# Optimization experiments

Hardware: AMD Instinct MI355X
Metric: run time of the kernel (lower is better)

Reference implementation:

```python
import jax, jax.numpy as jnp
import numpy as np

B, T, D, H, FF = 4, 2048, 1024, 16, 4096
HD = D // H
EPS = 1e-5


def layernorm(x, g, b):
    m = jnp.mean(x, axis=-1, keepdims=True)
    v = jnp.var(x, axis=-1, keepdims=True)
    return (x - m) * jax.lax.rsqrt(v + EPS) * g + b


def setup_inputs() -> dict:
    key = jax.random.key(0)
    ks = jax.random.split(key, 12)
    s = lambda fan_in: 1.0 / np.sqrt(fan_in)
    x = jax.random.normal(ks[0], (B, T, D), dtype=jnp.float32)
    mask = jnp.tril(jnp.ones((T, T), dtype=jnp.int32))[None, None]  # [1,1,T,T] causal
    return {
        "x": x,
        "mask": mask,
        "ln1_g": jnp.ones((D,), jnp.float32),
        "ln1_b": jnp.zeros((D,), jnp.float32),
        "ln2_g": jnp.ones((D,), jnp.float32),
        "ln2_b": jnp.zeros((D,), jnp.float32),
        "qkv_w": jax.random.normal(ks[1], (D, 3 * D), jnp.float32) * s(D),
        "out_w": jax.random.normal(ks[2], (D, D), jnp.float32) * s(D),
        "out_b": jnp.zeros((D,), jnp.float32),
        "fc1_w": jax.random.normal(ks[3], (D, FF), jnp.float32) * s(D),
        "fc1_b": jnp.zeros((FF,), jnp.float32),
        "fc2_w": jax.random.normal(ks[4], (FF, D), jnp.float32) * s(FF),
        "fc2_b": jnp.zeros((D,), jnp.float32),
    }


def reference(x, mask, ln1_g, ln1_b, ln2_g, ln2_b, qkv_w, out_w, out_b,
              fc1_w, fc1_b, fc2_w, fc2_b):
    # --- attention sublayer (pre-LN) ---
    h = layernorm(x, ln1_g, ln1_b)
    qkv = h @ qkv_w  # [B,T,3D]
    q, k, v = jnp.split(qkv, 3, axis=-1)
    q = q.reshape(B, T, H, HD).transpose(0, 2, 1, 3)  # [B,H,T,hd]
    k = k.reshape(B, T, H, HD).transpose(0, 2, 1, 3)
    v = v.reshape(B, T, H, HD).transpose(0, 2, 1, 3)
    scale = 1.0 / np.sqrt(HD)
    scores = jnp.einsum('bhqd,bhkd->bhqk', q, k) * scale  # [B,H,T,T]
    scores = jnp.where(mask == 0, -jnp.inf, scores)
    attn = jax.nn.softmax(scores, axis=-1)
    o = jnp.einsum('bhqk,bhkd->bhqd', attn, v)
    o = o.transpose(0, 2, 1, 3).reshape(B, T, D)
    x = x + (o @ out_w + out_b)
    # --- MLP sublayer (pre-LN) ---
    h = layernorm(x, ln2_g, ln2_b)
    h = jax.nn.gelu(h @ fc1_w + fc1_b, approximate=False)
    x = x + (h @ fc2_w + fc2_b)
    return x
```

## Files before the change

### kernel.cpp

```cpp
#include <hip/hip_runtime.h>

typedef unsigned short bfraw;
typedef __attribute__((ext_vector_type(8))) short short8;
typedef __attribute__((ext_vector_type(4))) float f32x4;

__device__ __forceinline__ float b2f(bfraw u){ return __uint_as_float(((unsigned int)u)<<16); }
__device__ __forceinline__ bfraw f2b(float f){
  unsigned int u = __float_as_uint(f);
  return (bfraw)((u + 0x7FFFu + ((u>>16)&1u)) >> 16);
}
__device__ __forceinline__ void store_out(float* p, float v){ *p = v; }
__device__ __forceinline__ void store_out(bfraw* p, float v){ *p = f2b(v); }
__device__ __forceinline__ void gload_lds16(const bfraw* g, short* l) {
  __builtin_amdgcn_global_load_lds((const __attribute__((address_space(1))) void*)g,
                                   (__attribute__((address_space(3))) void*)l, 16, 0, 0);
}
__device__ __forceinline__ unsigned int cvt_pk_bf16(float a, float b) {
  unsigned int r;
  asm("v_cvt_pk_bf16_f32 %0, %1, %2" : "=v"(r) : "v"(a), "v"(b));
  return r;
}

__global__ __launch_bounds__(1024) void transpose_f32_bf16(const float* __restrict__ in,
                                                           bfraw* __restrict__ out,
                                                           int R, int C) {
  __shared__ bfraw tile[64][65];
  const int tx = threadIdx.x, ty = threadIdx.y;
  const int c0 = blockIdx.x*64, r0 = blockIdx.y*64;
  #pragma unroll
  for (int u = 0; u < 4; ++u)
    tile[ty + u*16][tx] = f2b(in[(size_t)(r0 + ty + u*16)*C + c0 + tx]);
  __syncthreads();
  #pragma unroll
  for (int u = 0; u < 4; ++u)
    out[(size_t)(c0 + ty + u*16)*R + r0 + tx] = tile[tx][ty + u*16];
}

__global__ __launch_bounds__(256) void ln_kernel(const float* __restrict__ x,
                                                 const float* __restrict__ g,
                                                 const float* __restrict__ b,
                                                 bfraw* __restrict__ out) {
  const int row = blockIdx.x, tid = threadIdx.x;
  const f32x4 v = ((const f32x4*)(x + (size_t)row*1024))[tid];
  float s  = v[0]+v[1]+v[2]+v[3];
  float s2 = v[0]*v[0]+v[1]*v[1]+v[2]*v[2]+v[3]*v[3];
  #pragma unroll
  for (int off = 1; off < 64; off <<= 1) { s += __shfl_xor(s, off); s2 += __shfl_xor(s2, off); }
  __shared__ float red[8];
  const int wv = tid>>6, ln_ = tid&63;
  if (ln_ == 0) { red[wv] = s; red[4+wv] = s2; }
  __syncthreads();
  float a  = red[0]+red[1]+red[2]+red[3];
  float a2 = red[4]+red[5]+red[6]+red[7];
  float mean = a*(1.0f/1024.0f);
  float var  = a2*(1.0f/1024.0f) - mean*mean;
  float inv  = rsqrtf(var + 1e-5f);
  const f32x4 gr = ((const f32x4*)g)[tid];
  const f32x4 br = ((const f32x4*)b)[tid];
  ushort4 o4;
  o4.x = f2b((v[0]-mean)*inv*gr[0] + br[0]);
  o4.y = f2b((v[1]-mean)*inv*gr[1] + br[1]);
  o4.z = f2b((v[2]-mean)*inv*gr[2] + br[2]);
  o4.w = f2b((v[3]-mean)*inv*gr[3] + br[3]);
  ((ushort4*)(out + (size_t)row*1024))[tid] = o4;
}

template<int EPI, typename OutT>
__global__ __launch_bounds__(256) void gemm_bt(const bfraw* __restrict__ A,
                                               const bfraw* __restrict__ Bt,
                                               const float* __restrict__ bias,
                                               const float* __restrict__ resid,
                                               OutT* __restrict__ C,
                                               int M, int N, int K) {
  __shared__ __align__(16) short As[128*32];
  __shared__ __align__(16) short Bs[128*32];
  const int tid = threadIdx.x;
  const int wave = tid>>6, lane = tid&63;
  const int wm = wave>>1, wn = wave&1;
  const int q = lane>>4, r = lane&15;
  const int bm = blockIdx.x, bn = blockIdx.y;

  const int m0 = tid>>2, c0 = tid&3;
  const bfraw* Ag0 = A  + (size_t)(bm*128      + m0)*K + c0*8;
  const bfraw* Ag1 = A  + (size_t)(bm*128 + 64 + m0)*K + c0*8;
  const bfraw* Bg0 = Bt + (size_t)(bn*128      + m0)*K + c0*8;
  const bfraw* Bg1 = Bt + (size_t)(bn*128 + 64 + m0)*K + c0*8;
  short* Al0 = &As[tid*8];
  short* Al1 = &As[(256+tid)*8];
  short* Bl0 = &Bs[tid*8];
  short* Bl1 = &Bs[(256+tid)*8];

  f32x4 acc[4][4];
  #pragma unroll
  for (int mi = 0; mi < 4; ++mi)
    #pragma unroll
    for (int ni = 0; ni < 4; ++ni)
      acc[mi][ni] = (f32x4){0.f, 0.f, 0.f, 0.f};

  for (int k0 = 0; k0 < K; k0 += 32) {
    __syncthreads();
    gload_lds16(Ag0 + k0, Al0);
    gload_lds16(Ag1 + k0, Al1);
    gload_lds16(Bg0 + k0, Bl0);
    gload_lds16(Bg1 + k0, Bl1);
    __syncthreads();
    short8 af[4], bfr[4];
    #pragma unroll
    for (int mi = 0; mi < 4; ++mi)
      af[mi] = *(const short8*)&As[(wm*64 + mi*16 + r)*32 + q*8];
    #pragma unroll
    for (int ni = 0; ni < 4; ++ni)
      bfr[ni] = *(const short8*)&Bs[(wn*64 + ni*16 + r)*32 + q*8];
    #pragma unroll
    for (int mi = 0; mi < 4; ++mi)
      #pragma unroll
      for (int ni = 0; ni < 4; ++ni)
        acc[mi][ni] = __builtin_amdgcn_mfma_f32_16x16x32_bf16(af[mi], bfr[ni], acc[mi][ni], 0, 0, 0);
  }

  #pragma unroll
  for (int mi = 0; mi < 4; ++mi) {
    #pragma unroll
    for (int ni = 0; ni < 4; ++ni) {
      const int gcol = bn*128 + wn*64 + ni*16 + r;
      float bv = 0.f;
      if constexpr (EPI != 0) bv = bias[gcol];
      #pragma unroll
      for (int rg = 0; rg < 4; ++rg) {
        const int grow = bm*128 + wm*64 + mi*16 + q*4 + rg;
        float val = acc[mi][ni][rg];
        if constexpr (EPI != 0) val += bv;
        if constexpr (EPI == 2) val = 0.5f*val*(1.0f + erff(val*0.70710678118654752f));
        if constexpr (EPI == 1) val += resid[(size_t)grow*N + gcol];
        store_out(&C[(size_t)grow*N + gcol], val);
      }
    }
  }
}

__global__ __launch_bounds__(256) void flash_attn(const bfraw* __restrict__ qkv,
                                                  bfraw* __restrict__ o) {
  __shared__ __align__(16) short Ksh[4096];
  __shared__ __align__(16) short Vts[4096];
  __shared__ __align__(16) short Psh[4096];
  const int tid = threadIdx.x;
  const int w = tid >> 6, lane = tid & 63;
  const int r = lane & 15, qd = lane >> 4;
  const int bb = blockIdx.y >> 4, h = blockIdx.y & 15;
  const size_t hb = (size_t)bb * 2048;
  short* Pw = &Psh[w * 1024];
  const int f0 = tid, f1 = tid + 256;
  const int key0 = f0 >> 3, dc0 = (f0 & 7) * 8;
  const int key1 = f1 >> 3, dc1 = (f1 & 7) * 8;

  for (int pass = 0; pass < 2; ++pass) {
    const int qt = pass ? (31 - (int)blockIdx.x) : (int)blockIdx.x;
    const int q0 = qt * 64;
    const int ntile = qt + 1;

    short8 qf[2];
    {
      const bfraw* qrow = qkv + (hb + q0 + w*16 + r) * 3072 + h*64;
      qf[0] = *(const short8*)(qrow + qd*8);
      qf[1] = *(const short8*)(qrow + qd*8 + 32);
    }

    f32x4 oacc[4];
    #pragma unroll
    for (int nt = 0; nt < 4; ++nt) oacc[nt] = (f32x4){0.f,0.f,0.f,0.f};
    float m_i = -3.0e38f;
    float l_i = 0.f;

    short8 kpre[2], vpre[2];
    {
      const bfraw* b0 = qkv + (hb + key0) * 3072 + h*64 + dc0;
      const bfraw* b1 = qkv + (hb + key1) * 3072 + h*64 + dc1;
      kpre[0] = *(const short8*)(b0 + 1024); vpre[0] = *(const short8*)(b0 + 2048);
      kpre[1] = *(const short8*)(b1 + 1024); vpre[1] = *(const short8*)(b1 + 2048);
    }

    for (int t = 0; t < ntile; ++t) {
      __syncthreads();
      #pragma unroll
      for (int pz = 0; pz < 2; ++pz) {
        const int key = pz ? key1 : key0, dc = pz ? dc1 : dc0;
        *(short8*)&Ksh[key*64 + ((((dc>>3) ^ (key>>3)) & 7) << 3)] = kpre[pz];
        const int kg = key >> 3, k7 = key & 7, dg = dc >> 3;
        #pragma unroll
        for (int i2 = 0; i2 < 8; ++i2)
          Vts[(dc + i2)*64 + (((kg ^ dg) & 7) << 3) + k7] = vpre[pz][i2];
      }
      __syncthreads();
      if (t + 1 < ntile) {
        const int j0n = (t + 1) * 64;
        const bfraw* b0 = qkv + (hb + j0n + key0) * 3072 + h*64 + dc0;
        const bfraw* b1 = qkv + (hb + j0n + key1) * 3072 + h*64 + dc1;
        kpre[0] = *(const short8*)(b0 + 1024); vpre[0] = *(const short8*)(b0 + 2048);
        kpre[1] = *(const short8*)(b1 + 1024); vpre[1] = *(const short8*)(b1 + 2048);
      }

      f32x4 s4[4];
      __builtin_amdgcn_s_setprio(1);
      #pragma unroll
      for (int kt = 0; kt < 4; ++kt) {
        f32x4 a = (f32x4){0.f,0.f,0.f,0.f};
        const int key = kt*16 + r, kgk = key >> 3;
        #pragma unroll
        for (int ks = 0; ks < 2; ++ks) {
          short8 kf8 = *(const short8*)&Ksh[key*64 + ((((qd + ks*4) ^ kgk) & 7) << 3)];
          a = __builtin_amdgcn_mfma_f32_16x16x32_bf16(kf8, qf[ks], a, 0, 0, 0);
        }
        s4[kt] = a;
      }
      __builtin_amdgcn_s_setprio(0);

      const bool diag = (t == qt);
      #pragma unroll
      for (int kt = 0; kt < 4; ++kt)
        #pragma unroll
        for (int rg = 0; rg < 4; ++rg) {
          float v = s4[kt][rg] * 0.125f;
          if (diag && (kt*16 + qd*4 + rg > w*16 + r)) v = -3.0e38f;
          s4[kt][rg] = v;
        }

      float mx = s4[0][0];
      #pragma unroll
      for (int kt = 0; kt < 4; ++kt)
        #pragma unroll
        for (int rg = 0; rg < 4; ++rg) mx = fmaxf(mx, s4[kt][rg]);
      mx = fmaxf(mx, __shfl_xor(mx, 16));
      mx = fmaxf(mx, __shfl_xor(mx, 32));
      const float mn = fmaxf(m_i, mx);
      const float alpha = __expf(m_i - mn);
      m_i = mn;
      l_i *= alpha;

      float lsum = 0.f;
      #pragma unroll
      for (int kt = 0; kt < 4; ++kt) {
        const float p0 = __expf(s4[kt][0] - mn);
        const float p1 = __expf(s4[kt][1] - mn);
        const float p2 = __expf(s4[kt][2] - mn);
        const float p3 = __expf(s4[kt][3] - mn);
        lsum += (p0 + p1) + (p2 + p3);
        uint2 pk;
        pk.x = cvt_pk_bf16(p0, p1);
        pk.y = cvt_pk_bf16(p2, p3);
        *(uint2*)((char*)Pw + r*128 + ((((kt*2 + (qd>>1)) ^ (r&7)) & 7) << 4) + ((qd&1)<<3)) = pk;
      }
      lsum += __shfl_xor(lsum, 16);
      lsum += __shfl_xor(lsum, 32);
      l_i += lsum;
      #pragma unroll
      for (int nt = 0; nt < 4; ++nt)
        #pragma unroll
        for (int rg = 0; rg < 4; ++rg) oacc[nt][rg] *= alpha;

      short8 pf[2];
      #pragma unroll
      for (int ks = 0; ks < 2; ++ks)
        pf[ks] = *(const short8*)&Pw[r*64 + ((((qd + ks*4) ^ (r & 7)) & 7) << 3)];
      __builtin_amdgcn_s_setprio(1);
      #pragma unroll
      for (int nt = 0; nt < 4; ++nt) {
        const int d = nt*16 + r, dg = d >> 3;
        #pragma unroll
        for (int ks = 0; ks < 2; ++ks) {
          short8 vf = *(const short8*)&Vts[d*64 + ((((qd + ks*4) ^ dg) & 7) << 3)];
          oacc[nt] = __builtin_amdgcn_mfma_f32_16x16x32_bf16(vf, pf[ks], oacc[nt], 0, 0, 0);
        }
      }
      __builtin_amdgcn_s_setprio(0);
    }

    const float invl = 1.0f / l_i;
    bfraw* orow = o + (hb + q0 + w*16 + r) * 1024 + h*64;
    #pragma unroll
    for (int nt = 0; nt < 4; ++nt) {
      uint2 ov;
      ov.x = cvt_pk_bf16(oacc[nt][0]*invl, oacc[nt][1]*invl);
      ov.y = cvt_pk_bf16(oacc[nt][2]*invl, oacc[nt][3]*invl);
      *(uint2*)(orow + nt*16 + qd*4) = ov;
    }
  }
}

extern "C" void kernel_launch(void* const* d_in, const int* in_sizes, int n_in,
                              void* d_out, int out_size, void* d_ws, size_t ws_size,
                              hipStream_t stream) {
  (void)in_sizes; (void)n_in;
  const float* x    = (const float*)d_in[0];
  const float* ln1g = (const float*)d_in[2];
  const float* ln1b = (const float*)d_in[3];
  const float* ln2g = (const float*)d_in[4];
  const float* ln2b = (const float*)d_in[5];
  const float* qkvw = (const float*)d_in[6];
  const float* outw = (const float*)d_in[7];
  const float* outb = (const float*)d_in[8];
  const float* fc1w = (const float*)d_in[9];
  const float* fc1b = (const float*)d_in[10];
  const float* fc2w = (const float*)d_in[11];
  const float* fc2b = (const float*)d_in[12];
  float* out = (float*)d_out;

  char* ws = (char*)d_ws;
  size_t off = 0;
  auto alloc = [&](size_t bytes) -> void* { void* p = ws + off; off += (bytes + 255) & ~(size_t)255; return p; };
  bfraw* wt_qkv = (bfraw*)alloc(3072ULL*1024*2);
  bfraw* wt_out = (bfraw*)alloc(1024ULL*1024*2);
  bfraw* wt_fc1 = (bfraw*)alloc(4096ULL*1024*2);
  bfraw* wt_fc2 = (bfraw*)alloc(1024ULL*4096*2);
  bfraw* hbuf   = (bfraw*)alloc(8192ULL*1024*2);
  float* x1     = (float*)alloc(8192ULL*1024*4);
  char*  big    = (char*) alloc(8192ULL*3072*2 + 8192ULL*1024*2);
  bfraw* qkv  = (bfraw*)big;
  bfraw* obuf = (bfraw*)(big + 8192ULL*3072*2);
  bfraw* hf   = (bfraw*)big;

  if (off > ws_size) {
    (void)hipMemsetAsync(d_out, 0x7F, (size_t)out_size*4, stream);
    return;
  }

  dim3 tb(64, 16);
  transpose_f32_bf16<<<dim3(48, 16), tb, 0, stream>>>(qkvw, wt_qkv, 1024, 3072);
  transpose_f32_bf16<<<dim3(16, 16), tb, 0, stream>>>(outw, wt_out, 1024, 1024);
  transpose_f32_bf16<<<dim3(64, 16), tb, 0, stream>>>(fc1w, wt_fc1, 1024, 4096);
  transpose_f32_bf16<<<dim3(16, 64), tb, 0, stream>>>(fc2w, wt_fc2, 4096, 1024);

  ln_kernel<<<8192, 256, 0, stream>>>(x, ln1g, ln1b, hbuf);
  gemm_bt<0, bfraw><<<dim3(64, 24), 256, 0, stream>>>(hbuf, wt_qkv, nullptr, nullptr, qkv, 8192, 3072, 1024);
  flash_attn<<<dim3(16, 64), 256, 0, stream>>>(qkv, obuf);
  gemm_bt<1, float><<<dim3(64, 8), 256, 0, stream>>>(obuf, wt_out, outb, x, x1, 8192, 1024, 1024);
  ln_kernel<<<8192, 256, 0, stream>>>(x1, ln2g, ln2b, hbuf);
  gemm_bt<2, bfraw><<<dim3(64, 32), 256, 0, stream>>>(hbuf, wt_fc1, fc1b, nullptr, hf, 8192, 4096, 1024);
  gemm_bt<1, float><<<dim3(64, 8), 256, 0, stream>>>(hf, wt_fc2, fc2b, x1, out, 8192, 1024, 4096);
}
```

Measured before the change: 591.4 us.

## Replace GEMM with 256x256 double-buffered, swizzled, prefetching MFMA kernel

Replaces the 128x128 single-buffered GEMM with a 256x256-tile kernel that uses 512 threads, double-buffered LDS holding 64-wide K chunks, XOR-swizzled LDS layout and a block-id remap across 8 groups. Global-to-LDS loads for the next tile are issued between MFMA phases, with vmcnt waits and raised wave priority during MFMA, so memory latency overlaps with compute. Larger tiles raise data reuse, but grid sizes become small (128 blocks for the N=1024 GEMMs), which may leave CUs idle, and LDS use per block grows considerably.

```diff
diff --git a/kernel.cpp b/kernel.cpp
--- a/kernel.cpp
+++ b/kernel.cpp
@@ -19,6 +19,13 @@
   unsigned int r;
   asm("v_cvt_pk_bf16_f32 %0, %1, %2" : "=v"(r) : "v"(a), "v"(b));
   return r;
+}
+__device__ __forceinline__ void waitvm4(){ asm volatile("s_waitcnt vmcnt(4)" ::: "memory"); }
+__device__ __forceinline__ void waitvm0(){ asm volatile("s_waitcnt vmcnt(0)" ::: "memory"); }
+__device__ __forceinline__ void fence_bar(){
+  __builtin_amdgcn_sched_barrier(0);
+  __builtin_amdgcn_s_barrier();
+  __builtin_amdgcn_sched_barrier(0);
 }
 
 __global__ __launch_bounds__(1024) void transpose_f32_bf16(const float* __restrict__ in,
@@ -66,68 +73,149 @@
 }
 
 template<int EPI, typename OutT>
-__global__ __launch_bounds__(256) void gemm_bt(const bfraw* __restrict__ A,
-                                               const bfraw* __restrict__ Bt,
-                                               const float* __restrict__ bias,
-                                               const float* __restrict__ resid,
-                                               OutT* __restrict__ C,
-                                               int M, int N, int K) {
-  __shared__ __align__(16) short As[128*32];
-  __shared__ __align__(16) short Bs[128*32];
+__global__ __launch_bounds__(512, 2) void gemm256(const bfraw* __restrict__ A,
+                                                  const bfraw* __restrict__ Bt,
+                                                  const float* __restrict__ bias,
+                                                  const float* __restrict__ resid,
+                                                  OutT* __restrict__ C,
+                                                  int M, int N, int K) {
+  __shared__ __align__(16) short As[2*2*8192];
+  __shared__ __align__(16) short Bs[2*2*8192];
   const int tid = threadIdx.x;
-  const int wave = tid>>6, lane = tid&63;
-  const int wm = wave>>1, wn = wave&1;
-  const int q = lane>>4, r = lane&15;
-  const int bm = blockIdx.x, bn = blockIdx.y;
-
-  const int m0 = tid>>2, c0 = tid&3;
-  const bfraw* Ag0 = A  + (size_t)(bm*128      + m0)*K + c0*8;
-  const bfraw* Ag1 = A  + (size_t)(bm*128 + 64 + m0)*K + c0*8;
-  const bfraw* Bg0 = Bt + (size_t)(bn*128      + m0)*K + c0*8;
-  const bfraw* Bg1 = Bt + (size_t)(bn*128 + 64 + m0)*K + c0*8;
-  short* Al0 = &As[tid*8];
-  short* Al1 = &As[(256+tid)*8];
-  short* Bl0 = &Bs[tid*8];
-  short* Bl1 = &Bs[(256+tid)*8];
-
-  f32x4 acc[4][4];
+  const int wv = tid>>6, lane = tid&63;
+  const int wm = wv>>2, wn = wv&3;
+  const int q_ = lane>>4, r = lane&15;
+  const int nbm = M>>8, nbn = N>>8;
+  const int nwg = nbm*nbn;
+  int id = (int)blockIdx.x;
+  id = (id&7)*(nwg>>3) + (id>>3);
+  const int bm = id % nbm, bn = id / nbm;
+
+  const int srow = tid>>2, sch = tid&3;
+  const int sP   = (srow&3) ^ ((srow>>2)&1);
+  const int se   = ((sch ^ sP) << 3);
+  const bfraw* Ag = A  + (size_t)(bm*256 + srow)*K + se;
+  const bfraw* Bg = Bt + (size_t)(bn*256 + srow)*K + se;
+  const size_t rowstep = (size_t)128*K;
+
+  auto stageA = [&](int s, int k1, int nb) {
+    const bfraw* g = Ag + k1 + s*32;
+    short* d = As + (nb*2+s)*8192 + tid*8;
+    gload_lds16(g, d);
+    gload_lds16(g + rowstep, d + 4096);
+  };
+  auto stageB = [&](int s, int k1, int nb) {
+    const bfraw* g = Bg + k1 + s*32;
+    short* d = Bs + (nb*2+s)*8192 + tid*8;
+    gload_lds16(g, d);
+    gload_lds16(g + rowstep, d + 4096);
+  };
+
+  const int xsw = ((q_ ^ (r&3) ^ ((r>>2)&1)) << 3);
+  const int axo = (wm*128 + r)*32 + xsw;
+  const int bxo = (wn*64  + r)*32 + xsw;
+
+  f32x4 acc[8][4];
   #pragma unroll
-  for (int mi = 0; mi < 4; ++mi)
+  for (int mi = 0; mi < 8; ++mi)
     #pragma unroll
     for (int ni = 0; ni < 4; ++ni)
       acc[mi][ni] = (f32x4){0.f, 0.f, 0.f, 0.f};
 
-  for (int k0 = 0; k0 < K; k0 += 32) {
-    __syncthreads();
-    gload_lds16(Ag0 + k0, Al0);
-    gload_lds16(Ag1 + k0, Al1);
-    gload_lds16(Bg0 + k0, Bl0);
-    gload_lds16(Bg1 + k0, Bl1);
-    __syncthreads();
-    short8 af[4], bfr[4];
-    #pragma unroll
-    for (int mi = 0; mi < 4; ++mi)
-      af[mi] = *(const short8*)&As[(wm*64 + mi*16 + r)*32 + q*8];
-    #pragma unroll
-    for (int ni = 0; ni < 4; ++ni)
-      bfr[ni] = *(const short8*)&Bs[(wn*64 + ni*16 + r)*32 + q*8];
-    #pragma unroll
-    for (int mi = 0; mi < 4; ++mi)
+  stageA(0, 0, 0); stageB(0, 0, 0); stageA(1, 0, 0); stageB(1, 0, 0);
+  waitvm4();
+  fence_bar();
+
+  const int ntiles = K >> 6;
+  short8 af[4], bf[4];
+  for (int t = 0; t < ntiles; ++t) {
+    const int buf = t & 1, nb = buf ^ 1;
+    const int k1 = (t + 1) << 6;
+    const bool more = (t + 1) < ntiles;
+
+    {
+      const short* Ab = As + (buf*2+0)*8192;
+      const short* Bb = Bs + (buf*2+0)*8192;
+      #pragma unroll
+      for (int ni = 0; ni < 4; ++ni) bf[ni] = *(const short8*)&Bb[bxo + ni*512];
+      #pragma unroll
+      for (int m = 0; m < 4; ++m)   af[m]  = *(const short8*)&Ab[axo + m*512];
+    }
+    if (more) stageA(0, k1, nb);
+    fence_bar();
+    __builtin_amdgcn_s_setprio(1);
+    #pragma unroll
+    for (int m = 0; m < 4; ++m)
       #pragma unroll
       for (int ni = 0; ni < 4; ++ni)
-        acc[mi][ni] = __builtin_amdgcn_mfma_f32_16x16x32_bf16(af[mi], bfr[ni], acc[mi][ni], 0, 0, 0);
+        acc[m][ni] = __builtin_amdgcn_mfma_f32_16x16x32_bf16(af[m], bf[ni], acc[m][ni], 0, 0, 0);
+    __builtin_amdgcn_s_setprio(0);
+    fence_bar();
+
+    {
+      const short* Ab = As + (buf*2+0)*8192;
+      #pragma unroll
+      for (int m = 0; m < 4; ++m) af[m] = *(const short8*)&Ab[axo + (4+m)*512];
+    }
+    if (more) stageB(0, k1, nb);
+    if (more) waitvm4(); else waitvm0();
+    fence_bar();
+    __builtin_amdgcn_s_setprio(1);
+    #pragma unroll
+    for (int m = 0; m < 4; ++m)
+      #pragma unroll
+      for (int ni = 0; ni < 4; ++ni)
+        acc[4+m][ni] = __builtin_amdgcn_mfma_f32_16x16x32_bf16(af[m], bf[ni], acc[4+m][ni], 0, 0, 0);
+    __builtin_amdgcn_s_setprio(0);
+    fence_bar();
+
+    {
+      const short* Ab = As + (buf*2+1)*8192;
+      const short* Bb = Bs + (buf*2+1)*8192;
+      #pragma unroll
+      for (int ni = 0; ni < 4; ++ni) bf[ni] = *(const short8*)&Bb[bxo + ni*512];
+      #pragma unroll
+      for (int m = 0; m < 4; ++m)   af[m]  = *(const short8*)&Ab[axo + m*512];
+    }
+    if (more) stageA(1, k1, nb);
+    fence_bar();
+    __builtin_amdgcn_s_setprio(1);
+    #pragma unroll
+    for (int m = 0; m < 4; ++m)
+      #pragma unroll
+      for (int ni = 0; ni < 4; ++ni)
+        acc[m][ni] = __builtin_amdgcn_mfma_f32_16x16x32_bf16(af[m], bf[ni], acc[m][ni], 0, 0, 0);
+    __builtin_amdgcn_s_setprio(0);
+    fence_bar();
+
+    {
+      const short* Ab = As + (buf*2+1)*8192;
+      #pragma unroll
+      for (int m = 0; m < 4; ++m) af[m] = *(const short8*)&Ab[axo + (4+m)*512];
+    }
+    if (more) stageB(1, k1, nb);
+    if (more) waitvm4();
+    fence_bar();
+    __builtin_amdgcn_s_setprio(1);
+    #pragma unroll
+    for (int m = 0; m < 4; ++m)
+      #pragma unroll
+      for (int ni = 0; ni < 4; ++ni)
+        acc[4+m][ni] = __builtin_amdgcn_mfma_f32_16x16x32_bf16(af[m], bf[ni], acc[4+m][ni], 0, 0, 0);
+    __builtin_amdgcn_s_setprio(0);
+    fence_bar();
   }
 
   #pragma unroll
-  for (int mi = 0; mi < 4; ++mi) {
+  for (int mi = 0; mi < 8; ++mi) {
     #pragma unroll
     for (int ni = 0; ni < 4; ++ni) {
-      const int gcol = bn*128 + wn*64 + ni*16 + r;
+      const int gcol = bn*256 + wn*64 + ni*16 + r;
       float bv = 0.f;
       if constexpr (EPI != 0) bv = bias[gcol];
       #pragma unroll
       for (int rg = 0; rg < 4; ++rg) {
-        const int grow = bm*128 + wm*64 + mi*16 + q*4 + rg;
+        const int grow = bm*256 + wm*128 + mi*16 + q_*4 + rg;
         float val = acc[mi][ni][rg];
         if constexpr (EPI != 0) val += bv;
         if constexpr (EPI == 2) val = 0.5f*val*(1.0f + erff(val*0.70710678118654752f));
@@ -330,10 +418,10 @@
   transpose_f32_bf16<<<dim3(16, 64), tb, 0, stream>>>(fc2w, wt_fc2, 4096, 1024);
 
   ln_kernel<<<8192, 256, 0, stream>>>(x, ln1g, ln1b, hbuf);
-  gemm_bt<0, bfraw><<<dim3(64, 24), 256, 0, stream>>>(hbuf, wt_qkv, nullptr, nullptr, qkv, 8192, 3072, 1024);
+  gemm256<0, bfraw><<<dim3(384), 512, 0, stream>>>(hbuf, wt_qkv, nullptr, nullptr, qkv, 8192, 3072, 1024);
   flash_attn<<<dim3(16, 64), 256, 0, stream>>>(qkv, obuf);
-  gemm_bt<1, float><<<dim3(64, 8), 256, 0, stream>>>(obuf, wt_out, outb, x, x1, 8192, 1024, 1024);
+  gemm256<1, float><<<dim3(128), 512, 0, stream>>>(obuf, wt_out, outb, x, x1, 8192, 1024, 1024);
   ln_kernel<<<8192, 256, 0, stream>>>(x1, ln2g, ln2b, hbuf);
-  gemm_bt<2, bfraw><<<dim3(64, 32), 256, 0, stream>>>(hbuf, wt_fc1, fc1b, nullptr, hf, 8192, 4096, 1024);
-  gemm_bt<1, float><<<dim3(64, 8), 256, 0, stream>>>(hf, wt_fc2, fc2b, x1, out, 8192, 1024, 4096);
-}
+  gemm256<2, bfraw><<<dim3(512), 512, 0, stream>>>(hbuf, wt_fc1, fc1b, nullptr, hf, 8192, 4096, 1024);
+  gemm256<1, float><<<dim3(128), 512, 0, stream>>>(hf, wt_fc2, fc2b, x1, out, 8192, 1024, 4096);
+}
```

New measurement: 619.6 us. 1.05x slower.

## Rewrite GEMM with 256x128 tiles, double-buffered LDS, swizzle and XCD-aware block mapping

Applied to the files above, without the earlier changes.

Replaces the 128x128 single-buffered GEMM with a 512-thread 256x128-tile kernel. Global-to-LDS loads for the next 64-wide K tile are issued while MFMAs run on the current one, using explicit vmcnt waits, raw barriers and setprio. LDS addresses are XOR-swizzled to avoid bank conflicts, and the 1D grid is remapped so blocks are spread across the 8 XCDs. The larger tile raises data reuse and hides load latency, at the cost of more LDS, higher register pressure and hand-written synchronisation that is fragile to get right.

```diff
diff --git a/kernel.cpp b/kernel.cpp
--- a/kernel.cpp
+++ b/kernel.cpp
@@ -20,6 +20,8 @@
   asm("v_cvt_pk_bf16_f32 %0, %1, %2" : "=v"(r) : "v"(a), "v"(b));
   return r;
 }
+__device__ __forceinline__ void waitvm3(){ asm volatile("s_waitcnt vmcnt(3)" ::: "memory"); }
+__device__ __forceinline__ void waitvm0(){ asm volatile("s_waitcnt vmcnt(0)" ::: "memory"); }
 
 __global__ __launch_bounds__(1024) void transpose_f32_bf16(const float* __restrict__ in,
                                                            bfraw* __restrict__ out,
@@ -66,29 +68,44 @@
 }
 
 template<int EPI, typename OutT>
-__global__ __launch_bounds__(256) void gemm_bt(const bfraw* __restrict__ A,
-                                               const bfraw* __restrict__ Bt,
-                                               const float* __restrict__ bias,
-                                               const float* __restrict__ resid,
-                                               OutT* __restrict__ C,
-                                               int M, int N, int K) {
-  __shared__ __align__(16) short As[128*32];
-  __shared__ __align__(16) short Bs[128*32];
+__global__ __launch_bounds__(512, 2) void gemm_bn128(const bfraw* __restrict__ A,
+                                                     const bfraw* __restrict__ Bt,
+                                                     const float* __restrict__ bias,
+                                                     const float* __restrict__ resid,
+                                                     OutT* __restrict__ C,
+                                                     int M, int N, int K) {
+  __shared__ __align__(16) short As[2*2*8192];
+  __shared__ __align__(16) short Bs[2*2*4096];
   const int tid = threadIdx.x;
-  const int wave = tid>>6, lane = tid&63;
-  const int wm = wave>>1, wn = wave&1;
-  const int q = lane>>4, r = lane&15;
-  const int bm = blockIdx.x, bn = blockIdx.y;
-
-  const int m0 = tid>>2, c0 = tid&3;
-  const bfraw* Ag0 = A  + (size_t)(bm*128      + m0)*K + c0*8;
-  const bfraw* Ag1 = A  + (size_t)(bm*128 + 64 + m0)*K + c0*8;
-  const bfraw* Bg0 = Bt + (size_t)(bn*128      + m0)*K + c0*8;
-  const bfraw* Bg1 = Bt + (size_t)(bn*128 + 64 + m0)*K + c0*8;
-  short* Al0 = &As[tid*8];
-  short* Al1 = &As[(256+tid)*8];
-  short* Bl0 = &Bs[tid*8];
-  short* Bl1 = &Bs[(256+tid)*8];
+  const int wv = tid>>6, lane = tid&63;
+  const int wm = wv>>1, wn = wv&1;
+  const int q_ = lane>>4, r = lane&15;
+  const int nbm = M>>8, nbn = N>>7;
+  const int nwg = nbm*nbn;
+  int id = (int)blockIdx.x;
+  id = (id&7)*(nwg>>3) + (id>>3);
+  const int bm = id % nbm, bn = id / nbm;
+
+  const int srow = tid>>2, sch = tid&3;
+  const int sP   = (srow&3) ^ ((srow>>2)&1);
+  const int se   = ((sch ^ sP) << 3);
+  const bfraw* Ag = A  + (size_t)(bm*256 + srow)*K + se;
+  const bfraw* Bg = Bt + (size_t)(bn*128 + srow)*K + se;
+  const size_t rowstepA = (size_t)128*K;
+
+  auto stage = [&](int s, int k0s, int nb) {
+    const bfraw* ga = Ag + k0s + s*32;
+    short* da = As + (nb*2+s)*8192 + tid*8;
+    gload_lds16(ga, da);
+    gload_lds16(ga + rowstepA, da + 4096);
+    const bfraw* gb = Bg + k0s + s*32;
+    short* db = Bs + (nb*2+s)*4096 + tid*8;
+    gload_lds16(gb, db);
+  };
+
+  const int xsw = ((q_ ^ (r&3) ^ ((r>>2)&1)) << 3);
+  const int axo = (wm*64 + r)*32 + xsw;
+  const int bxo = (wn*64 + r)*32 + xsw;
 
   f32x4 acc[4][4];
   #pragma unroll
@@ -97,25 +114,55 @@
     for (int ni = 0; ni < 4; ++ni)
       acc[mi][ni] = (f32x4){0.f, 0.f, 0.f, 0.f};
 
-  for (int k0 = 0; k0 < K; k0 += 32) {
-    __syncthreads();
-    gload_lds16(Ag0 + k0, Al0);
-    gload_lds16(Ag1 + k0, Al1);
-    gload_lds16(Bg0 + k0, Bl0);
-    gload_lds16(Bg1 + k0, Bl1);
-    __syncthreads();
-    short8 af[4], bfr[4];
-    #pragma unroll
-    for (int mi = 0; mi < 4; ++mi)
-      af[mi] = *(const short8*)&As[(wm*64 + mi*16 + r)*32 + q*8];
-    #pragma unroll
-    for (int ni = 0; ni < 4; ++ni)
-      bfr[ni] = *(const short8*)&Bs[(wn*64 + ni*16 + r)*32 + q*8];
-    #pragma unroll
-    for (int mi = 0; mi < 4; ++mi)
+  stage(0, 0, 0); stage(1, 0, 0);
+  waitvm3();
+  __builtin_amdgcn_s_barrier();
+
+  const int ntiles = K >> 6;
+  short8 af[4], bf[4];
+  for (int t = 0; t < ntiles; ++t) {
+    const int buf = t & 1, nb = buf ^ 1;
+    const int k1 = (t + 1) << 6;
+    const bool more = (t + 1) < ntiles;
+
+    {
+      const short* Ab = As + (buf*2+0)*8192;
+      const short* Bb = Bs + (buf*2+0)*4096;
+      #pragma unroll
+      for (int ni = 0; ni < 4; ++ni) bf[ni] = *(const short8*)&Bb[bxo + ni*512];
+      #pragma unroll
+      for (int m = 0; m < 4; ++m)   af[m]  = *(const short8*)&Ab[axo + m*512];
+    }
+    if (more) stage(0, k1, nb);
+    if (more) waitvm3(); else waitvm0();
+    __builtin_amdgcn_s_barrier();
+    __builtin_amdgcn_s_setprio(1);
+    #pragma unroll
+    for (int m = 0; m < 4; ++m)
       #pragma unroll
       for (int ni = 0; ni < 4; ++ni)
-        acc[mi][ni] = __builtin_amdgcn_mfma_f32_16x16x32_bf16(af[mi], bfr[ni], acc[mi][ni], 0, 0, 0);
+        acc[m][ni] = __builtin_amdgcn_mfma_f32_16x16x32_bf16(af[m], bf[ni], acc[m][ni], 0, 0, 0);
+    __builtin_amdgcn_s_setprio(0);
+    __builtin_amdgcn_s_barrier();
+
+    {
+      const short* Ab = As + (buf*2+1)*8192;
+      const short* Bb = Bs + (buf*2+1)*4096;
+      #pragma unroll
+      for (int ni = 0; ni < 4; ++ni) bf[ni] = *(const short8*)&Bb[bxo + ni*512];
+      #pragma unroll
+      for (int m = 0; m < 4; ++m)   af[m]  = *(const short8*)&Ab[axo + m*512];
+    }
+    if (more) { stage(1, k1, nb); waitvm3(); }
+    __builtin_amdgcn_s_barrier();
+    __builtin_amdgcn_s_setprio(1);
+    #pragma unroll
+    for (int m = 0; m < 4; ++m)
+      #pragma unroll
+      for (int ni = 0; ni < 4; ++ni)
+        acc[m][ni] = __builtin_amdgcn_mfma_f32_16x16x32_bf16(af[m], bf[ni], acc[m][ni], 0, 0, 0);
+    __builtin_amdgcn_s_setprio(0);
+    __builtin_amdgcn_s_barrier();
   }
 
   #pragma unroll
@@ -127,7 +174,7 @@
       if constexpr (EPI != 0) bv = bias[gcol];
       #pragma unroll
       for (int rg = 0; rg < 4; ++rg) {
-        const int grow = bm*128 + wm*64 + mi*16 + q*4 + rg;
+        const int grow = bm*256 + wm*64 + mi*16 + q_*4 + rg;
         float val = acc[mi][ni][rg];
         if constexpr (EPI != 0) val += bv;
         if constexpr (EPI == 2) val = 0.5f*val*(1.0f + erff(val*0.70710678118654752f));
@@ -330,10 +377,10 @@
   transpose_f32_bf16<<<dim3(16, 64), tb, 0, stream>>>(fc2w, wt_fc2, 4096, 1024);
 
   ln_kernel<<<8192, 256, 0, stream>>>(x, ln1g, ln1b, hbuf);
-  gemm_bt<0, bfraw><<<dim3(64, 24), 256, 0, stream>>>(hbuf, wt_qkv, nullptr, nullptr, qkv, 8192, 3072, 1024);
+  gemm_bn128<0, bfraw><<<dim3(768), 512, 0, stream>>>(hbuf, wt_qkv, nullptr, nullptr, qkv, 8192, 3072, 1024);
   flash_attn<<<dim3(16, 64), 256, 0, stream>>>(qkv, obuf);
-  gemm_bt<1, float><<<dim3(64, 8), 256, 0, stream>>>(obuf, wt_out, outb, x, x1, 8192, 1024, 1024);
+  gemm_bn128<1, float><<<dim3(256), 512, 0, stream>>>(obuf, wt_out, outb, x, x1, 8192, 1024, 1024);
   ln_kernel<<<8192, 256, 0, stream>>>(x1, ln2g, ln2b, hbuf);
-  gemm_bt<2, bfraw><<<dim3(64, 32), 256, 0, stream>>>(hbuf, wt_fc1, fc1b, nullptr, hf, 8192, 4096, 1024);
-  gemm_bt<1, float><<<dim3(64, 8), 256, 0, stream>>>(hf, wt_fc2, fc2b, x1, out, 8192, 1024, 4096);
-}
+  gemm_bn128<2, bfraw><<<dim3(1024), 512, 0, stream>>>(hbuf, wt_fc1, fc1b, nullptr, hf, 8192, 4096, 1024);
+  gemm_bn128<1, float><<<dim3(256), 512, 0, stream>>>(hf, wt_fc2, fc2b, x1, out, 8192, 1024, 4096);
+}
```

Result: slower. 616.8 us (+4.3%).

## Double-buffer K/V tiles and widen flash-attention key chunks to 128

Applied to the files above, without the earlier changes.

Flash attention now processes 128 keys per iteration instead of 64. K and V tiles are double-buffered in LDS, with the next chunk written to LDS and the chunk after that prefetched into registers while the current one is computed. This halves the number of online-softmax rescales and removes one barrier per iteration, aiming to overlap loads with MFMA work. It costs more LDS and registers, which may lower occupancy. The diagonal chunk is now half-masked for even query tiles.

```diff
diff --git a/kernel.cpp b/kernel.cpp
--- a/kernel.cpp
+++ b/kernel.cpp
@@ -140,23 +140,24 @@
 
 __global__ __launch_bounds__(256) void flash_attn(const bfraw* __restrict__ qkv,
                                                   bfraw* __restrict__ o) {
-  __shared__ __align__(16) short Ksh[4096];
-  __shared__ __align__(16) short Vts[4096];
-  __shared__ __align__(16) short Psh[4096];
+  __shared__ __align__(16) short Ksh[2][8192];
+  __shared__ __align__(16) short Vts[2][8192];
+  __shared__ __align__(16) short Psh[4][2048];
   const int tid = threadIdx.x;
   const int w = tid >> 6, lane = tid & 63;
   const int r = lane & 15, qd = lane >> 4;
   const int bb = blockIdx.y >> 4, h = blockIdx.y & 15;
   const size_t hb = (size_t)bb * 2048;
-  short* Pw = &Psh[w * 1024];
-  const int f0 = tid, f1 = tid + 256;
-  const int key0 = f0 >> 3, dc0 = (f0 & 7) * 8;
-  const int key1 = f1 >> 3, dc1 = (f1 & 7) * 8;
+  short* Pw = &Psh[w][0];
+  const int skey = tid >> 3, sa = tid & 7, sdc = sa * 8, sk7 = skey & 7;
+  const int kposz = ((sa ^ sk7) & 7) << 3;
+
+  short8 kpre[4], vpre[4];
 
   for (int pass = 0; pass < 2; ++pass) {
     const int qt = pass ? (31 - (int)blockIdx.x) : (int)blockIdx.x;
     const int q0 = qt * 64;
-    const int ntile = qt + 1;
+    const int nchunk = (qt >> 1) + 1;
 
     short8 qf[2];
     {
@@ -171,62 +172,90 @@
     float m_i = -3.0e38f;
     float l_i = 0.f;
 
-    short8 kpre[2], vpre[2];
     {
-      const bfraw* b0 = qkv + (hb + key0) * 3072 + h*64 + dc0;
-      const bfraw* b1 = qkv + (hb + key1) * 3072 + h*64 + dc1;
-      kpre[0] = *(const short8*)(b0 + 1024); vpre[0] = *(const short8*)(b0 + 2048);
-      kpre[1] = *(const short8*)(b1 + 1024); vpre[1] = *(const short8*)(b1 + 2048);
-    }
-
-    for (int t = 0; t < ntile; ++t) {
-      __syncthreads();
-      #pragma unroll
-      for (int pz = 0; pz < 2; ++pz) {
-        const int key = pz ? key1 : key0, dc = pz ? dc1 : dc0;
-        *(short8*)&Ksh[key*64 + ((((dc>>3) ^ (key>>3)) & 7) << 3)] = kpre[pz];
-        const int kg = key >> 3, k7 = key & 7, dg = dc >> 3;
-        #pragma unroll
-        for (int i2 = 0; i2 < 8; ++i2)
-          Vts[(dc + i2)*64 + (((kg ^ dg) & 7) << 3) + k7] = vpre[pz][i2];
-      }
-      __syncthreads();
-      if (t + 1 < ntile) {
-        const int j0n = (t + 1) * 64;
-        const bfraw* b0 = qkv + (hb + j0n + key0) * 3072 + h*64 + dc0;
-        const bfraw* b1 = qkv + (hb + j0n + key1) * 3072 + h*64 + dc1;
-        kpre[0] = *(const short8*)(b0 + 1024); vpre[0] = *(const short8*)(b0 + 2048);
-        kpre[1] = *(const short8*)(b1 + 1024); vpre[1] = *(const short8*)(b1 + 2048);
-      }
-
-      f32x4 s4[4];
+      const bfraw* p0 = qkv + (hb + skey) * 3072 + h*64 + sdc;
+      #pragma unroll
+      for (int i = 0; i < 4; ++i) {
+        const bfraw* p = p0 + (size_t)i*32*3072;
+        kpre[i] = *(const short8*)(p + 1024);
+        vpre[i] = *(const short8*)(p + 2048);
+      }
+    }
+    __syncthreads();
+    #pragma unroll
+    for (int i = 0; i < 4; ++i) {
+      *(short8*)&Ksh[0][(32*i + skey)*64 + kposz] = kpre[i];
+      const int kg = 4*i + w;
+      #pragma unroll
+      for (int j = 0; j < 8; ++j)
+        Vts[0][(sdc + j)*128 + (((kg & 8) | ((kg ^ j ^ sa) & 7)) << 3) + sk7] = vpre[i][j];
+    }
+    if (nchunk > 1) {
+      const bfraw* p0 = qkv + (hb + 128 + skey) * 3072 + h*64 + sdc;
+      #pragma unroll
+      for (int i = 0; i < 4; ++i) {
+        const bfraw* p = p0 + (size_t)i*32*3072;
+        kpre[i] = *(const short8*)(p + 1024);
+        vpre[i] = *(const short8*)(p + 2048);
+      }
+    }
+    asm volatile("s_waitcnt lgkmcnt(0)" ::: "memory");
+    __builtin_amdgcn_s_barrier();
+
+    for (int t = 0; t < nchunk; ++t) {
+      const int buf = t & 1;
+      if (t + 1 < nchunk) {
+        const int nb = buf ^ 1;
+        #pragma unroll
+        for (int i = 0; i < 4; ++i) {
+          *(short8*)&Ksh[nb][(32*i + skey)*64 + kposz] = kpre[i];
+          const int kg = 4*i + w;
+          #pragma unroll
+          for (int j = 0; j < 8; ++j)
+            Vts[nb][(sdc + j)*128 + (((kg & 8) | ((kg ^ j ^ sa) & 7)) << 3) + sk7] = vpre[i][j];
+        }
+      }
+      if (t + 2 < nchunk) {
+        const bfraw* p0 = qkv + (hb + (t+2)*128 + skey) * 3072 + h*64 + sdc;
+        #pragma unroll
+        for (int i = 0; i < 4; ++i) {
+          const bfraw* p = p0 + (size_t)i*32*3072;
+          kpre[i] = *(const short8*)(p + 1024);
+          vpre[i] = *(const short8*)(p + 2048);
+        }
+      }
+
+      const short* Kb = &Ksh[buf][0];
+      const short* Vb = &Vts[buf][0];
+      f32x4 s4[8];
       __builtin_amdgcn_s_setprio(1);
       #pragma unroll
-      for (int kt = 0; kt < 4; ++kt) {
+      for (int kt = 0; kt < 8; ++kt) {
         f32x4 a = (f32x4){0.f,0.f,0.f,0.f};
-        const int key = kt*16 + r, kgk = key >> 3;
+        const int key = kt*16 + r;
         #pragma unroll
         for (int ks = 0; ks < 2; ++ks) {
-          short8 kf8 = *(const short8*)&Ksh[key*64 + ((((qd + ks*4) ^ kgk) & 7) << 3)];
+          short8 kf8 = *(const short8*)&Kb[key*64 + ((((qd + ks*4) ^ (r & 7)) & 7) << 3)];
           a = __builtin_amdgcn_mfma_f32_16x16x32_bf16(kf8, qf[ks], a, 0, 0, 0);
         }
         s4[kt] = a;
       }
       __builtin_amdgcn_s_setprio(0);
 
-      const bool diag = (t == qt);
-      #pragma unroll
-      for (int kt = 0; kt < 4; ++kt)
+      const bool diag = (t == nchunk - 1);
+      const int dqr = q0 + w*16 + r - t*128;
+      #pragma unroll
+      for (int kt = 0; kt < 8; ++kt)
         #pragma unroll
         for (int rg = 0; rg < 4; ++rg) {
           float v = s4[kt][rg] * 0.125f;
-          if (diag && (kt*16 + qd*4 + rg > w*16 + r)) v = -3.0e38f;
+          if (diag && (kt*16 + qd*4 + rg > dqr)) v = -3.0e38f;
           s4[kt][rg] = v;
         }
 
       float mx = s4[0][0];
       #pragma unroll
-      for (int kt = 0; kt < 4; ++kt)
+      for (int kt = 0; kt < 8; ++kt)
         #pragma unroll
         for (int rg = 0; rg < 4; ++rg) mx = fmaxf(mx, s4[kt][rg]);
       mx = fmaxf(mx, __shfl_xor(mx, 16));
@@ -238,7 +267,7 @@
 
       float lsum = 0.f;
       #pragma unroll
-      for (int kt = 0; kt < 4; ++kt) {
+      for (int kt = 0; kt < 8; ++kt) {
         const float p0 = __expf(s4[kt][0] - mn);
         const float p1 = __expf(s4[kt][1] - mn);
         const float p2 = __expf(s4[kt][2] - mn);
@@ -247,7 +276,9 @@
         uint2 pk;
         pk.x = cvt_pk_bf16(p0, p1);
         pk.y = cvt_pk_bf16(p2, p3);
-        *(uint2*)((char*)Pw + r*128 + ((((kt*2 + (qd>>1)) ^ (r&7)) & 7) << 4) + ((qd&1)<<3)) = pk;
+        const int c = 2*kt + (qd >> 1);
+        const int pos = (c & 8) | ((c ^ (r & 7)) & 7);
+        *(uint2*)((char*)Pw + r*256 + (pos << 4) + ((qd & 1) << 3)) = pk;
       }
       lsum += __shfl_xor(lsum, 16);
       lsum += __shfl_xor(lsum, 32);
@@ -257,21 +288,30 @@
         #pragma unroll
         for (int rg = 0; rg < 4; ++rg) oacc[nt][rg] *= alpha;
 
-      short8 pf[2];
-      #pragma unroll
-      for (int ks = 0; ks < 2; ++ks)
-        pf[ks] = *(const short8*)&Pw[r*64 + ((((qd + ks*4) ^ (r & 7)) & 7) << 3)];
+      short8 pf[4];
+      #pragma unroll
+      for (int ks = 0; ks < 4; ++ks) {
+        const int c = 4*ks + qd;
+        const int pos = (c & 8) | ((c ^ (r & 7)) & 7);
+        pf[ks] = *(const short8*)&Pw[r*128 + (pos << 3)];
+      }
       __builtin_amdgcn_s_setprio(1);
       #pragma unroll
       for (int nt = 0; nt < 4; ++nt) {
-        const int d = nt*16 + r, dg = d >> 3;
-        #pragma unroll
-        for (int ks = 0; ks < 2; ++ks) {
-          short8 vf = *(const short8*)&Vts[d*64 + ((((qd + ks*4) ^ dg) & 7) << 3)];
+        const int d = nt*16 + r;
+        const int dx = (r & 7) ^ ((d >> 3) & 7);
+        #pragma unroll
+        for (int ks = 0; ks < 4; ++ks) {
+          const int c = qd + 4*ks;
+          const int pos = (c & 8) | ((c ^ dx) & 7);
+          short8 vf = *(const short8*)&Vb[d*128 + (pos << 3)];
           oacc[nt] = __builtin_amdgcn_mfma_f32_16x16x32_bf16(vf, pf[ks], oacc[nt], 0, 0, 0);
         }
       }
       __builtin_amdgcn_s_setprio(0);
+
+      asm volatile("s_waitcnt lgkmcnt(0)" ::: "memory");
+      __builtin_amdgcn_s_barrier();
     }
 
     const float invl = 1.0f / l_i;
```

Measured after the change: 661.8 us. 11.9% more time.
